# Performance work log

Measured on AMD Instinct MI355X. Metric: run time of the kernel, lower is better.

## Reference

```python
import jax, jax.numpy as jnp
import numpy as np

HID = 4096
H = 32
DK = 128
DV = 128
QKV = H * DK * 2 + H * DV  # 12288
EPS = 1e-06


def setup_inputs() -> dict:
    key = jax.random.key(0)
    ks = jax.random.split(key, 12)
    s = 0.02
    return {
        "hidden_states": jax.random.normal(ks[0], (1, 1, HID), jnp.float32),
        "delta_state": jax.random.normal(ks[1], (1, H, DV, DK), jnp.float32) * 0.1,
        "conv_state": jax.random.normal(ks[2], (1, QKV, 1, 3), jnp.float32),
        "W_qkv": jax.random.normal(ks[3], (QKV, HID), jnp.float32) * s,
        "W_z": jax.random.normal(ks[4], (H * DV, HID), jnp.float32) * s,
        "W_a": jax.random.normal(ks[5], (H, HID), jnp.float32) * s,
        "W_b": jax.random.normal(ks[6], (H, HID), jnp.float32) * s,
        "W_out": jax.random.normal(ks[7], (HID, H * DV), jnp.float32) * s,
        "conv_w": jax.random.normal(ks[8], (1, QKV, 1, 4), jnp.float32) * 0.01,
        "A_log": jnp.zeros((H,), jnp.float32),
        "dt_bias": jnp.zeros((H,), jnp.float32),
        "rms_weight": jnp.ones((DV,), jnp.float32),
    }


def reference(hidden_states, delta_state, conv_state, W_qkv, W_z, W_a, W_b,
              W_out, conv_w, A_log, dt_bias, rms_weight):
    hs = hidden_states[0, 0]                       # [HID]
    qkv = W_qkv @ hs                               # [QKV]
    z = W_z @ hs                                   # [H*DV]
    a = W_a @ hs                                   # [H]
    b = W_b @ hs                                   # [H]

    # manual causal conv1d decode step
    cs = conv_state[0, :, 0, :]                    # [QKV, 3]
    w = conv_w[0, :, 0, :]                         # [QKV, 4]
    conv_out = (w[:, :3] * cs).sum(-1) + w[:, 3] * qkv
    new_conv_state = jnp.concatenate([cs[:, 1:], qkv[:, None]], axis=-1)[None, :, None, :]

    qkv_act = jax.nn.silu(conv_out)
    q = qkv_act[: H * DK].reshape(H, DK)
    k = qkv_act[H * DK: 2 * H * DK].reshape(H, DK)
    v = qkv_act[2 * H * DK:].reshape(H, DV)

    # L2 normalize q, k over head dim (eps inside rsqrt), then scale q
    q = q * jax.lax.rsqrt(jnp.sum(q * q, axis=-1, keepdims=True) + 1e-06)
    k = k * jax.lax.rsqrt(jnp.sum(k * k, axis=-1, keepdims=True) + 1e-06)
    q = q * (1.0 / np.sqrt(DK))

    beta = jax.nn.sigmoid(b)                       # [H]
    gate = -jnp.exp(A_log) * jax.nn.softplus(a + dt_bias)  # [H]

    # delta-rule state update (transposed storage [H, DV, DK])
    S = delta_state[0]
    S = jnp.exp(gate)[:, None, None] * S
    retrieved = jnp.einsum('hvk,hk->hv', S, k)
    delta = beta[:, None] * (v - retrieved)
    S = S + jnp.einsum('hv,hk->hvk', delta, k)
    out = jnp.einsum('hvk,hk->hv', S, q)           # [H, DV]

    # GatedRMSNorm: RMSNorm(x) * weight * silu(z); layer_norm([x,-x]) == x/sqrt(mean(x^2)+eps)
    var = jnp.mean(out * out, axis=-1, keepdims=True)
    normed = out * jax.lax.rsqrt(var + EPS) * rms_weight
    out = normed * jax.nn.silu(z.reshape(H, DV))

    result = (W_out @ out.reshape(H * DV)).reshape(1, 1, HID)
    return result, S[None], new_conv_state
```

## Files before the change

### kernel.cpp

```cpp
#include <hip/hip_runtime.h>
#include <math.h>

#define HID 4096
#define NH 32
#define DK 128
#define DV 128
#define NQKV 12288
#define ROWS1 16448

#define OUT_S_OFF 4096
#define OUT_CONV_OFF 528384

#define WS_Z_OFF 12288
#define WS_A_OFF 16384
#define WS_B_OFF 16416
#define WS_O_OFF 16448

typedef float f32x4 __attribute__((ext_vector_type(4)));

__device__ __forceinline__ float wave_reduce_sum(float x) {
#pragma unroll
  for (int off = 32; off > 0; off >>= 1) x += __shfl_xor(x, off, 64);
  return x;
}

__device__ __forceinline__ float silu_f(float x) {
  return x / (1.f + __expf(-x));
}

__global__ __launch_bounds__(256) void k_matvec_in(
    const float* __restrict__ hs,
    const float* __restrict__ Wqkv, const float* __restrict__ Wz,
    const float* __restrict__ Wa, const float* __restrict__ Wb,
    const float* __restrict__ conv_state,
    float* __restrict__ ws, float* __restrict__ dout) {
  const int wave = threadIdx.x >> 6, lane = threadIdx.x & 63;
  const int row = blockIdx.x * 4 + wave;
  const float* W;
  int r;
  if (row < NQKV) { W = Wqkv; r = row; }
  else if (row < NQKV + HID) { W = Wz; r = row - NQKV; }
  else if (row < NQKV + HID + NH) { W = Wa; r = row - (NQKV + HID); }
  else { W = Wb; r = row - (NQKV + HID + NH); }
  const f32x4* __restrict__ Wr = (const f32x4*)(W + (size_t)r * HID);
  const f32x4* __restrict__ h4 = (const f32x4*)hs;
  float acc = 0.f;
#pragma unroll
  for (int j = 0; j < 16; ++j) {
    const f32x4 w = __builtin_nontemporal_load(&Wr[lane + j * 64]);
    const f32x4 h = h4[lane + j * 64];
    acc += w.x * h.x + w.y * h.y + w.z * h.z + w.w * h.w;
  }
  acc = wave_reduce_sum(acc);
  if (lane == 0) {
    ws[row] = acc;
    if (row < NQKV) {
      dout[OUT_CONV_OFF + row * 3 + 0] = conv_state[row * 3 + 1];
      dout[OUT_CONV_OFF + row * 3 + 1] = conv_state[row * 3 + 2];
      dout[OUT_CONV_OFF + row * 3 + 2] = acc;
    }
  }
}

__global__ __launch_bounds__(256) void k_state(
    const float* __restrict__ delta_state, const float* __restrict__ conv_state,
    const float* __restrict__ conv_w, const float* __restrict__ A_log,
    const float* __restrict__ dt_bias,
    float* __restrict__ ws, float* __restrict__ dout) {
  const int bid = blockIdx.x;
  const int h = bid >> 5;
  const int vbase = (bid & 31) * 4;
  const int t = threadIdx.x;
  __shared__ __align__(16) float qn[DK];
  __shared__ __align__(16) float kn[DK];
  __shared__ float va4[4];
  __shared__ float s_eg, s_beta, s_kq, s_rq, s_rk;

  {
    const int seg = t >> 7, li = t & 127;
    const int row = seg * 4096 + h * 128 + li;
    const float c0 = conv_state[row * 3 + 0];
    const float c1 = conv_state[row * 3 + 1];
    const float c2 = conv_state[row * 3 + 2];
    const float w0 = conv_w[row * 4 + 0], w1 = conv_w[row * 4 + 1];
    const float w2 = conv_w[row * 4 + 2], w3 = conv_w[row * 4 + 3];
    const float co = w0 * c0 + w1 * c1 + w2 * c2 + w3 * ws[row];
    const float act = silu_f(co);
    if (seg == 0) qn[li] = act; else kn[li] = act;
  }
  if (t < 4) {
    const int row = 2 * 4096 + h * 128 + vbase + t;
    const float c0 = conv_state[row * 3 + 0];
    const float c1 = conv_state[row * 3 + 1];
    const float c2 = conv_state[row * 3 + 2];
    const float w0 = conv_w[row * 4 + 0], w1 = conv_w[row * 4 + 1];
    const float w2 = conv_w[row * 4 + 2], w3 = conv_w[row * 4 + 3];
    va4[t] = silu_f(w0 * c0 + w1 * c1 + w2 * c2 + w3 * ws[row]);
  }
  if (t == 4) {
    const float aa = ws[WS_A_OFF + h] + dt_bias[h];
    s_eg = __expf(-__expf(A_log[h]) * log1pf(__expf(aa)));
    s_beta = 1.f / (1.f + __expf(-ws[WS_B_OFF + h]));
  }
  __syncthreads();

  if (t < 64) {
    const float q0 = qn[t], q1 = qn[t + 64];
    const float k0 = kn[t], k1 = kn[t + 64];
    float sq = q0 * q0 + q1 * q1;
    float sk = k0 * k0 + k1 * k1;
    float dq = q0 * k0 + q1 * k1;
#pragma unroll
    for (int off = 32; off > 0; off >>= 1) {
      sq += __shfl_xor(sq, off, 64);
      sk += __shfl_xor(sk, off, 64);
      dq += __shfl_xor(dq, off, 64);
    }
    if (t == 0) {
      const float rq = rsqrtf(sq + 1e-6f) * 0.08838834764831845f;
      const float rk = rsqrtf(sk + 1e-6f);
      s_rq = rq; s_rk = rk;
      s_kq = dq * rq * rk;
    }
  }
  __syncthreads();
  if (t < 128) { qn[t] *= s_rq; kn[t] *= s_rk; }
  __syncthreads();

  const int w = t >> 6, lane = t & 63;
  const int v = vbase + w;
  const size_t roff = ((size_t)h * DV + v) * DK;
  const float2 s2 = ((const float2*)(delta_state + roff))[lane];
  const float2 kk = ((const float2*)kn)[lane];
  const float2 qq = ((const float2*)qn)[lane];
  float r1 = s2.x * kk.x + s2.y * kk.y;
  float r2 = s2.x * qq.x + s2.y * qq.y;
#pragma unroll
  for (int off = 32; off > 0; off >>= 1) {
    r1 += __shfl_xor(r1, off, 64);
    r2 += __shfl_xor(r2, off, 64);
  }
  const float eg = s_eg;
  const float dv_ = s_beta * (va4[w] - eg * r1);
  const float o = eg * r2 + dv_ * s_kq;
  float2 out2;
  out2.x = eg * s2.x + dv_ * kk.x;
  out2.y = eg * s2.y + dv_ * kk.y;
  ((float2*)(dout + OUT_S_OFF + roff))[lane] = out2;
  if (lane == 0) ws[WS_O_OFF + h * DV + v] = o;
}

__global__ __launch_bounds__(256) void k_matvec_out(
    const float* __restrict__ Wout, const float* __restrict__ rms_w,
    float* __restrict__ ws, float* __restrict__ dout) {
  __shared__ __align__(16) float g[HID];
  __shared__ float scale[NH];
  const int t = threadIdx.x;
#pragma unroll
  for (int j = 0; j < 16; ++j) g[j * 256 + t] = ws[WS_O_OFF + j * 256 + t];
  __syncthreads();
  if (t < 32) {
    float ssum = 0.f;
#pragma unroll 4
    for (int v = 0; v < 128; ++v) {
      const float o = g[t * 128 + ((v + t) & 127)];
      ssum += o * o;
    }
    scale[t] = rsqrtf(ssum * (1.f / 128.f) + 1e-6f);
  }
  __syncthreads();
#pragma unroll
  for (int j = 0; j < 16; ++j) {
    const int idx = j * 256 + t;
    const int hh = idx >> 7, vv = idx & 127;
    const float zv = ws[WS_Z_OFF + idx];
    g[idx] = g[idx] * scale[hh] * rms_w[vv] * silu_f(zv);
  }
  __syncthreads();

  const int wave = t >> 6, lane = t & 63;
  const int row = blockIdx.x * 4 + wave;
  const f32x4* __restrict__ Wr = (const f32x4*)(Wout + (size_t)row * HID);
  const f32x4* __restrict__ g4 = (const f32x4*)g;
  float acc = 0.f;
#pragma unroll
  for (int j = 0; j < 16; ++j) {
    const f32x4 w = __builtin_nontemporal_load(&Wr[lane + j * 64]);
    const f32x4 gg = g4[lane + j * 64];
    acc += w.x * gg.x + w.y * gg.y + w.z * gg.z + w.w * gg.w;
  }
  acc = wave_reduce_sum(acc);
  if (lane == 0) dout[row] = acc;
}

extern "C" void kernel_launch(void* const* d_in, const int* in_sizes, int n_in,
                              void* d_out, int out_size, void* d_ws, size_t ws_size,
                              hipStream_t stream) {
  const float* hs         = (const float*)d_in[0];
  const float* delta_state= (const float*)d_in[1];
  const float* conv_state = (const float*)d_in[2];
  const float* Wqkv       = (const float*)d_in[3];
  const float* Wz         = (const float*)d_in[4];
  const float* Wa         = (const float*)d_in[5];
  const float* Wb         = (const float*)d_in[6];
  const float* Wout       = (const float*)d_in[7];
  const float* conv_w     = (const float*)d_in[8];
  const float* A_log      = (const float*)d_in[9];
  const float* dt_bias    = (const float*)d_in[10];
  const float* rms_w      = (const float*)d_in[11];
  float* ws  = (float*)d_ws;
  float* out = (float*)d_out;

  k_matvec_in<<<ROWS1 / 4, 256, 0, stream>>>(hs, Wqkv, Wz, Wa, Wb, conv_state,
                                             ws, out);
  k_state<<<NH * 32, 256, 0, stream>>>(delta_state, conv_state, conv_w, A_log,
                                       dt_bias, ws, out);
  k_matvec_out<<<HID / 4, 256, 0, stream>>>(Wout, rms_w, ws, out);
}
```

Measured before the change: 65.41 us.

## Stage hidden vector in LDS, split accumulators, vectorize norm prologue, nontemporal state IO

The input matvec now copies the hidden-state vector into shared memory once per block, and both matvecs use two independent accumulators. The delta-state kernel switches to nontemporal loads and stores for the state rows. The output kernel's RMS-norm prologue is rebuilt with vectorized global reads and a shuffle-based per-head sum of squares, replacing the serial per-thread loop over shared memory. Together these aim to cut redundant global traffic and prologue latency, at the cost of an extra barrier and LDS use in the first kernel.

Measured after the change: 64.41 us. About the same (-1.5%).

```diff
diff --git a/kernel.cpp b/kernel.cpp
--- a/kernel.cpp
+++ b/kernel.cpp
@@ -17,6 +17,7 @@
 #define WS_O_OFF 16448
 
 typedef float f32x4 __attribute__((ext_vector_type(4)));
+typedef float f32x2 __attribute__((ext_vector_type(2)));
 
 __device__ __forceinline__ float wave_reduce_sum(float x) {
 #pragma unroll
@@ -34,6 +35,16 @@
     const float* __restrict__ Wa, const float* __restrict__ Wb,
     const float* __restrict__ conv_state,
     float* __restrict__ ws, float* __restrict__ dout) {
+  __shared__ __align__(16) float hls[HID];
+  {
+    f32x4* hl4 = (f32x4*)hls;
+    const f32x4* h4 = (const f32x4*)hs;
+#pragma unroll
+    for (int m = 0; m < 4; ++m)
+      hl4[m * 256 + threadIdx.x] = h4[m * 256 + threadIdx.x];
+  }
+  __syncthreads();
+
   const int wave = threadIdx.x >> 6, lane = threadIdx.x & 63;
   const int row = blockIdx.x * 4 + wave;
   const float* W;
@@ -43,15 +54,18 @@
   else if (row < NQKV + HID + NH) { W = Wa; r = row - (NQKV + HID); }
   else { W = Wb; r = row - (NQKV + HID + NH); }
   const f32x4* __restrict__ Wr = (const f32x4*)(W + (size_t)r * HID);
-  const f32x4* __restrict__ h4 = (const f32x4*)hs;
-  float acc = 0.f;
-#pragma unroll
-  for (int j = 0; j < 16; ++j) {
-    const f32x4 w = __builtin_nontemporal_load(&Wr[lane + j * 64]);
-    const f32x4 h = h4[lane + j * 64];
-    acc += w.x * h.x + w.y * h.y + w.z * h.z + w.w * h.w;
-  }
-  acc = wave_reduce_sum(acc);
+  const f32x4* __restrict__ hl4 = (const f32x4*)hls;
+  float acc0 = 0.f, acc1 = 0.f;
+#pragma unroll
+  for (int j = 0; j < 16; j += 2) {
+    const f32x4 w0 = __builtin_nontemporal_load(&Wr[lane + j * 64]);
+    const f32x4 h0 = hl4[lane + j * 64];
+    const f32x4 w1 = __builtin_nontemporal_load(&Wr[lane + (j + 1) * 64]);
+    const f32x4 h1 = hl4[lane + (j + 1) * 64];
+    acc0 += w0.x * h0.x + w0.y * h0.y + w0.z * h0.z + w0.w * h0.w;
+    acc1 += w1.x * h1.x + w1.y * h1.y + w1.z * h1.z + w1.w * h1.w;
+  }
+  float acc = wave_reduce_sum(acc0 + acc1);
   if (lane == 0) {
     ws[row] = acc;
     if (row < NQKV) {
@@ -130,9 +144,9 @@
   const int w = t >> 6, lane = t & 63;
   const int v = vbase + w;
   const size_t roff = ((size_t)h * DV + v) * DK;
-  const float2 s2 = ((const float2*)(delta_state + roff))[lane];
-  const float2 kk = ((const float2*)kn)[lane];
-  const float2 qq = ((const float2*)qn)[lane];
+  const f32x2 s2 = __builtin_nontemporal_load(&((const f32x2*)(delta_state + roff))[lane]);
+  const f32x2 kk = ((const f32x2*)kn)[lane];
+  const f32x2 qq = ((const f32x2*)qn)[lane];
   float r1 = s2.x * kk.x + s2.y * kk.y;
   float r2 = s2.x * qq.x + s2.y * qq.y;
 #pragma unroll
@@ -143,10 +157,10 @@
   const float eg = s_eg;
   const float dv_ = s_beta * (va4[w] - eg * r1);
   const float o = eg * r2 + dv_ * s_kq;
-  float2 out2;
+  f32x2 out2;
   out2.x = eg * s2.x + dv_ * kk.x;
   out2.y = eg * s2.y + dv_ * kk.y;
-  ((float2*)(dout + OUT_S_OFF + roff))[lane] = out2;
+  __builtin_nontemporal_store(out2, &((f32x2*)(dout + OUT_S_OFF + roff))[lane]);
   if (lane == 0) ws[WS_O_OFF + h * DV + v] = o;
 }
 
@@ -156,25 +170,38 @@
   __shared__ __align__(16) float g[HID];
   __shared__ float scale[NH];
   const int t = threadIdx.x;
-#pragma unroll
-  for (int j = 0; j < 16; ++j) g[j * 256 + t] = ws[WS_O_OFF + j * 256 + t];
-  __syncthreads();
-  if (t < 32) {
-    float ssum = 0.f;
-#pragma unroll 4
-    for (int v = 0; v < 128; ++v) {
-      const float o = g[t * 128 + ((v + t) & 127)];
-      ssum += o * o;
-    }
-    scale[t] = rsqrtf(ssum * (1.f / 128.f) + 1e-6f);
-  }
-  __syncthreads();
-#pragma unroll
-  for (int j = 0; j < 16; ++j) {
-    const int idx = j * 256 + t;
-    const int hh = idx >> 7, vv = idx & 127;
-    const float zv = ws[WS_Z_OFF + idx];
-    g[idx] = g[idx] * scale[hh] * rms_w[vv] * silu_f(zv);
+  {
+    const int hh = t >> 3, sub = t & 7;
+    const f32x4* o4 = (const f32x4*)(ws + WS_O_OFF + hh * 128 + sub * 16);
+    float ss = 0.f;
+#pragma unroll
+    for (int j = 0; j < 4; ++j) {
+      const f32x4 o = o4[j];
+      ss += o.x * o.x + o.y * o.y + o.z * o.z + o.w * o.w;
+    }
+    ss += __shfl_xor(ss, 1, 64);
+    ss += __shfl_xor(ss, 2, 64);
+    ss += __shfl_xor(ss, 4, 64);
+    if (sub == 0) scale[hh] = rsqrtf(ss * (1.f / 128.f) + 1e-6f);
+  }
+  __syncthreads();
+  {
+    const f32x4* o4 = (const f32x4*)(ws + WS_O_OFF);
+    const f32x4* z4 = (const f32x4*)(ws + WS_Z_OFF);
+    const f32x4* r4 = (const f32x4*)rms_w;
+    f32x4* g4 = (f32x4*)g;
+#pragma unroll
+    for (int j = 0; j < 4; ++j) {
+      const int i = j * 256 + t;
+      const f32x4 o = o4[i], z = z4[i], r = r4[i & 31];
+      const float sc = scale[i >> 5];
+      f32x4 gg;
+      gg.x = o.x * sc * r.x * silu_f(z.x);
+      gg.y = o.y * sc * r.y * silu_f(z.y);
+      gg.z = o.z * sc * r.z * silu_f(z.z);
+      gg.w = o.w * sc * r.w * silu_f(z.w);
+      g4[i] = gg;
+    }
   }
   __syncthreads();
 
@@ -182,14 +209,17 @@
   const int row = blockIdx.x * 4 + wave;
   const f32x4* __restrict__ Wr = (const f32x4*)(Wout + (size_t)row * HID);
   const f32x4* __restrict__ g4 = (const f32x4*)g;
-  float acc = 0.f;
-#pragma unroll
-  for (int j = 0; j < 16; ++j) {
-    const f32x4 w = __builtin_nontemporal_load(&Wr[lane + j * 64]);
-    const f32x4 gg = g4[lane + j * 64];
-    acc += w.x * gg.x + w.y * gg.y + w.z * gg.z + w.w * gg.w;
-  }
-  acc = wave_reduce_sum(acc);
+  float acc0 = 0.f, acc1 = 0.f;
+#pragma unroll
+  for (int j = 0; j < 16; j += 2) {
+    const f32x4 w0 = __builtin_nontemporal_load(&Wr[lane + j * 64]);
+    const f32x4 gg0 = g4[lane + j * 64];
+    const f32x4 w1 = __builtin_nontemporal_load(&Wr[lane + (j + 1) * 64]);
+    const f32x4 gg1 = g4[lane + (j + 1) * 64];
+    acc0 += w0.x * gg0.x + w0.y * gg0.y + w0.z * gg0.z + w0.w * gg0.w;
+    acc1 += w1.x * gg1.x + w1.y * gg1.y + w1.z * gg1.z + w1.w * gg1.w;
+  }
+  const float acc = wave_reduce_sum(acc0 + acc1);
   if (lane == 0) dout[row] = acc;
 }
 
```
